# Optimization experiments

Measured on AMD Instinct MI355X. Metric: run time of the kernel, lower is better.

Reference implementation:

```python
import jax, jax.numpy as jnp
import numpy as np

B, C, H, W = 8, 16, 64, 64
O = 32
K = 3
STRIDE = 1
HO = (H - K) // STRIDE + 1  # 62
WO = (W - K) // STRIDE + 1  # 62
BIAS_VAL = 0.1


def setup_inputs() -> dict:
    key = jax.random.key(0)
    k1, k2 = jax.random.split(key)
    x = jax.random.normal(k1, (B, C, H, W), dtype=jnp.float32)
    # per-location weights: (1, O, C, Ho, Wo, K*K) in torch; drop leading 1
    weight = jax.random.normal(k2, (O, C, HO, WO, K * K), dtype=jnp.float32)
    bias = jnp.full((1, O, HO, WO), BIAS_VAL, dtype=jnp.float32)
    return {"x": x, "weight": weight, "bias": bias}


def _extract_patches(x):
    # emulate x.unfold(2,K,S).unfold(3,K,S).reshape(..., K*K)
    # patch index k = ki*K + kj
    patches = [
        x[:, :, ki:ki + (HO - 1) * STRIDE + 1:STRIDE, kj:kj + (WO - 1) * STRIDE + 1:STRIDE]
        for ki in range(K) for kj in range(K)
    ]
    return jnp.stack(patches, axis=-1)  # [B, C, Ho, Wo, K*K]


def reference(x, weight, bias):
    patches = _extract_patches(x)  # [B, C, Ho, Wo, K2]
    # (x.unsqueeze(1) * weight).sum([2, -1]) == contraction over C and K2 per location
    out = jnp.einsum('bchwk,ochwk->bohw', patches, weight)
    return out + bias
```

## Files before the change

### kernel.cpp

```cpp
#include <hip/hip_runtime.h>


#define BB 8
#define CC 16
#define HH 64
#define WW 64
#define OO 32
#define HO 62
#define WO 62
#define NLOC (HO * WO)
#define TOTAL (OO * NLOC)

typedef float f4 __attribute__((ext_vector_type(4)));
typedef float f2 __attribute__((ext_vector_type(2)));

__device__ __forceinline__ void async_f32_to_lds(const float* g, float* l) {
  __builtin_amdgcn_global_load_lds((const __attribute__((address_space(1))) void*)g,
                                   (__attribute__((address_space(3))) void*)l,
                                   4, 0, 0);
}
__device__ __forceinline__ void async_f32x4_to_lds(const float* g, float* l) {
  __builtin_amdgcn_global_load_lds((const __attribute__((address_space(1))) void*)g,
                                   (__attribute__((address_space(3))) void*)l,
                                   16, 0, 0);
}

__global__ __launch_bounds__(256) void lc2d_kernel(
    const float* __restrict__ x, const float* __restrict__ weight,
    const float* __restrict__ bias, float* __restrict__ out) {
  __shared__ __align__(16) float smem[4 * 2 * 576];

  const int tid  = threadIdx.x;
  const int lane = tid & 63;
  const int wave = tid >> 6;
  const int l = lane & 15;
  const int q = lane >> 4;
  const int ho = blockIdx.x % HO;
  const int o  = blockIdx.x / HO;

  float* buf0 = smem + wave * 1152;

  const int colbase = 4 * l;
  const int f2off = (l < 15) ? 4 : -4;

  const float* wbase = weight + (size_t)(o * CC + wave * 4) * (NLOC * 9)
                              + (size_t)ho * (WO * 9);

#define STAGE(SRC, DST)                                              \
  {                                                                  \
    async_f32x4_to_lds((SRC) + lane * 4, (DST));                     \
    async_f32x4_to_lds((SRC) + 256 + lane * 4, (DST) + 256);         \
    if (lane < 46) async_f32_to_lds((SRC) + 512 + lane, (DST) + 512);\
  }

  STAGE(wbase, buf0)

  f4 acc[2];
  acc[0] = (f4)0.f;
  acc[1] = (f4)0.f;

#pragma unroll
  for (int cc = 0; cc < 4; ++cc) {
    const float* cur = buf0 + (cc & 1) * 576;
    float* nxt = buf0 + ((cc + 1) & 1) * 576;
    const int c = wave * 4 + cc;

    __builtin_amdgcn_sched_barrier(0);
    f4 v4[2][3];
    f2 v2[2][3];
#pragma unroll
    for (int bo = 0; bo < 2; ++bo) {
      const float* xb = x + ((size_t)(2 * q + bo) * CC + c) * (HH * WW)
                          + (size_t)ho * WW + colbase;
#pragma unroll
      for (int r = 0; r < 3; ++r) {
        v4[bo][r] = *(const f4*)(xb + r * WW);
        v2[bo][r] = *(const f2*)(xb + r * WW + f2off);
      }
    }
    __builtin_amdgcn_sched_barrier(0);
    if (cc < 3) {
      const float* wg = wbase + (size_t)(cc + 1) * (NLOC * 9);
      STAGE(wg, nxt)
    }
    __builtin_amdgcn_sched_barrier(0);
    if (cc < 3) {
      asm volatile("s_waitcnt vmcnt(15)");
    } else {
      asm volatile("s_waitcnt vmcnt(12)");
    }
    __builtin_amdgcn_sched_barrier(0);

    f4 wq[9];
#pragma unroll
    for (int k = 0; k < 9; ++k)
      wq[k] = *(const f4*)(cur + 36 * l + 4 * k);

#pragma unroll
    for (int bo = 0; bo < 2; ++bo) {
#pragma unroll
      for (int w4 = 0; w4 < 4; ++w4) {
        float s = 0.f;
#pragma unroll
        for (int r = 0; r < 3; ++r) {
#pragma unroll
          for (int j = 0; j < 3; ++j) {
            const int e = w4 + j;
            const int wi = w4 * 9 + r * 3 + j;
            const float xv = (e < 4) ? v4[bo][r][e] : v2[bo][r][e - 4];
            s += xv * wq[wi >> 2][wi & 3];
          }
        }
        acc[bo][w4] += s;
      }
    }
  }
#undef STAGE

#pragma unroll
  for (int bo = 0; bo < 2; ++bo)
    *(f4*)(buf0 + (2 * q + bo) * 64 + colbase) = acc[bo];
  __syncthreads();

  for (int p = tid; p < 512; p += 256) {
    const int b  = p >> 6;
    const int wo = p & 63;
    if (wo < WO) {
      float s = smem[0 * 1152 + p] + smem[1 * 1152 + p]
              + smem[2 * 1152 + p] + smem[3 * 1152 + p];
      const int loc = o * NLOC + ho * WO + wo;
      out[(size_t)b * TOTAL + loc] = s + bias[loc];
    }
  }
}

extern "C" void kernel_launch(void* const* d_in, const int* in_sizes, int n_in,
                              void* d_out, int out_size, void* d_ws, size_t ws_size,
                              hipStream_t stream) {
  const float* x = (const float*)d_in[0];
  const float* w = (const float*)d_in[1];
  const float* bias = (const float*)d_in[2];
  float* out = (float*)d_out;

  hipLaunchKernelGGL(lc2d_kernel, dim3(OO * HO), dim3(256), 0, stream,
                     x, w, bias, out);
}
```

Before: 26.22 us.

## Process four output channels per block to reuse input loads

```diff
diff --git a/kernel.cpp b/kernel.cpp
--- a/kernel.cpp
+++ b/kernel.cpp
@@ -8,6 +8,7 @@
 #define OO 32
 #define HO 62
 #define WO 62
+#define OG 4
 #define NLOC (HO * WO)
 #define TOTAL (OO * NLOC)
 
@@ -28,7 +29,7 @@
 __global__ __launch_bounds__(256) void lc2d_kernel(
     const float* __restrict__ x, const float* __restrict__ weight,
     const float* __restrict__ bias, float* __restrict__ out) {
-  __shared__ __align__(16) float smem[4 * 2 * 576];
+  __shared__ __align__(16) float smem[4 * 2 * OG * 576];
 
   const int tid  = threadIdx.x;
   const int lane = tid & 63;
@@ -36,33 +37,42 @@
   const int l = lane & 15;
   const int q = lane >> 4;
   const int ho = blockIdx.x % HO;
-  const int o  = blockIdx.x / HO;
+  const int og = blockIdx.x / HO;
 
-  float* buf0 = smem + wave * 1152;
+  float* wbuf = smem + wave * (2 * OG * 576);
 
   const int colbase = 4 * l;
   const int f2off = (l < 15) ? 4 : -4;
 
-  const float* wbase = weight + (size_t)(o * CC + wave * 4) * (NLOC * 9)
+  const float* wbase = weight + ((size_t)(og * OG) * CC + wave * 4) * (NLOC * 9)
                               + (size_t)ho * (WO * 9);
 
-#define STAGE(SRC, DST)                                              \
-  {                                                                  \
-    async_f32x4_to_lds((SRC) + lane * 4, (DST));                     \
-    async_f32x4_to_lds((SRC) + 256 + lane * 4, (DST) + 256);         \
-    if (lane < 46) async_f32_to_lds((SRC) + 512 + lane, (DST) + 512);\
+#define STAGE_ROW(SRC, DST)                                            \
+  {                                                                    \
+    async_f32x4_to_lds((SRC) + lane * 4, (DST));                       \
+    async_f32x4_to_lds((SRC) + 256 + lane * 4, (DST) + 256);           \
+    if (lane < 46) async_f32_to_lds((SRC) + 512 + lane, (DST) + 512);  \
+  }
+#define STAGE_BODY(cc, DST)                                            \
+  {                                                                    \
+    _Pragma("unroll")                                                  \
+    for (int oo = 0; oo < OG; ++oo)                                    \
+      STAGE_ROW(wbase + ((size_t)oo * CC + (cc)) * (NLOC * 9),         \
+                (DST) + oo * 576);                                     \
   }
 
-  STAGE(wbase, buf0)
+  STAGE_BODY(0, wbuf)
 
-  f4 acc[2];
-  acc[0] = (f4)0.f;
-  acc[1] = (f4)0.f;
+  f4 acc[2][OG];
+#pragma unroll
+  for (int bo = 0; bo < 2; ++bo)
+#pragma unroll
+    for (int oo = 0; oo < OG; ++oo) acc[bo][oo] = (f4)0.f;
 
 #pragma unroll
   for (int cc = 0; cc < 4; ++cc) {
-    const float* cur = buf0 + (cc & 1) * 576;
-    float* nxt = buf0 + ((cc + 1) & 1) * 576;
+    const float* cur = wbuf + (cc & 1) * (OG * 576);
+    float* nxt = wbuf + ((cc + 1) & 1) * (OG * 576);
     const int c = wave * 4 + cc;
 
     __builtin_amdgcn_sched_barrier(0);
@@ -79,56 +89,60 @@
       }
     }
     __builtin_amdgcn_sched_barrier(0);
-    if (cc < 3) {
-      const float* wg = wbase + (size_t)(cc + 1) * (NLOC * 9);
-      STAGE(wg, nxt)
-    }
+    if (cc < 3) STAGE_BODY(cc + 1, nxt)
     __builtin_amdgcn_sched_barrier(0);
     if (cc < 3) {
-      asm volatile("s_waitcnt vmcnt(15)");
+      asm volatile("s_waitcnt vmcnt(24)");
     } else {
       asm volatile("s_waitcnt vmcnt(12)");
     }
     __builtin_amdgcn_sched_barrier(0);
 
-    f4 wq[9];
 #pragma unroll
-    for (int k = 0; k < 9; ++k)
-      wq[k] = *(const f4*)(cur + 36 * l + 4 * k);
+    for (int oo = 0; oo < OG; ++oo) {
+      f4 wq[9];
+#pragma unroll
+      for (int k = 0; k < 9; ++k)
+        wq[k] = *(const f4*)(cur + oo * 576 + 36 * l + 4 * k);
 
 #pragma unroll
-    for (int bo = 0; bo < 2; ++bo) {
+      for (int bo = 0; bo < 2; ++bo) {
 #pragma unroll
-      for (int w4 = 0; w4 < 4; ++w4) {
-        float s = 0.f;
+        for (int w4 = 0; w4 < 4; ++w4) {
+          float s = 0.f;
 #pragma unroll
-        for (int r = 0; r < 3; ++r) {
+          for (int r = 0; r < 3; ++r) {
 #pragma unroll
-          for (int j = 0; j < 3; ++j) {
-            const int e = w4 + j;
-            const int wi = w4 * 9 + r * 3 + j;
-            const float xv = (e < 4) ? v4[bo][r][e] : v2[bo][r][e - 4];
-            s += xv * wq[wi >> 2][wi & 3];
+            for (int j = 0; j < 3; ++j) {
+              const int e = w4 + j;
+              const int wi = w4 * 9 + r * 3 + j;
+              const float xv = (e < 4) ? v4[bo][r][e] : v2[bo][r][e - 4];
+              s += xv * wq[wi >> 2][wi & 3];
+            }
           }
+          acc[bo][oo][w4] += s;
         }
-        acc[bo][w4] += s;
       }
     }
   }
-#undef STAGE
+#undef STAGE_BODY
+#undef STAGE_ROW
 
 #pragma unroll
-  for (int bo = 0; bo < 2; ++bo)
-    *(f4*)(buf0 + (2 * q + bo) * 64 + colbase) = acc[bo];
+  for (int oo = 0; oo < OG; ++oo)
+#pragma unroll
+    for (int bo = 0; bo < 2; ++bo)
+      *(f4*)(wbuf + (oo * 8 + 2 * q + bo) * 64 + colbase) = acc[bo][oo];
   __syncthreads();
 
-  for (int p = tid; p < 512; p += 256) {
-    const int b  = p >> 6;
+  for (int p = tid; p < OG * 8 * 64; p += 256) {
+    const int oo = p >> 9;
+    const int b  = (p >> 6) & 7;
     const int wo = p & 63;
     if (wo < WO) {
-      float s = smem[0 * 1152 + p] + smem[1 * 1152 + p]
-              + smem[2 * 1152 + p] + smem[3 * 1152 + p];
-      const int loc = o * NLOC + ho * WO + wo;
+      float s = smem[0 * 4608 + p] + smem[1 * 4608 + p]
+              + smem[2 * 4608 + p] + smem[3 * 4608 + p];
+      const int loc = (og * OG + oo) * NLOC + ho * WO + wo;
       out[(size_t)b * TOTAL + loc] = s + bias[loc];
     }
   }
@@ -142,6 +156,6 @@
   const float* bias = (const float*)d_in[2];
   float* out = (float*)d_out;
 
-  hipLaunchKernelGGL(lc2d_kernel, dim3(OO * HO), dim3(256), 0, stream,
+  hipLaunchKernelGGL(lc2d_kernel, dim3((OO / OG) * HO), dim3(256), 0, stream,
                      x, w, bias, out);
 }
```

Result: slower. 30.17 us (+15.0%).

## Split channels over eight waves and stage all weights into LDS up front

Applied to the files above, without the earlier changes.

```diff
diff --git a/kernel.cpp b/kernel.cpp
--- a/kernel.cpp
+++ b/kernel.cpp
@@ -25,10 +25,10 @@
                                    16, 0, 0);
 }
 
-__global__ __launch_bounds__(256) void lc2d_kernel(
+__global__ __launch_bounds__(512) void lc2d_kernel(
     const float* __restrict__ x, const float* __restrict__ weight,
     const float* __restrict__ bias, float* __restrict__ out) {
-  __shared__ __align__(16) float smem[4 * 2 * 576];
+  __shared__ __align__(16) float smem[CC * 576];
 
   const int tid  = threadIdx.x;
   const int lane = tid & 63;
@@ -38,59 +38,59 @@
   const int ho = blockIdx.x % HO;
   const int o  = blockIdx.x / HO;
 
-  float* buf0 = smem + wave * 1152;
-
   const int colbase = 4 * l;
   const int f2off = (l < 15) ? 4 : -4;
 
-  const float* wbase = weight + (size_t)(o * CC + wave * 4) * (NLOC * 9)
-                              + (size_t)ho * (WO * 9);
-
-#define STAGE(SRC, DST)                                              \
-  {                                                                  \
-    async_f32x4_to_lds((SRC) + lane * 4, (DST));                     \
-    async_f32x4_to_lds((SRC) + 256 + lane * 4, (DST) + 256);         \
-    if (lane < 46) async_f32_to_lds((SRC) + 512 + lane, (DST) + 512);\
+  if (wave == 0) {
+    const float* wb = weight + ((size_t)o * CC * NLOC + (size_t)ho * WO) * 9;
+#pragma unroll
+    for (int c = 0; c < CC; ++c) {
+      const float* src = wb + (size_t)c * (NLOC * 9);
+      float* dst = smem + c * 576;
+      async_f32x4_to_lds(src + lane * 4, dst);
+      async_f32x4_to_lds(src + 256 + lane * 4, dst + 256);
+      if (lane < 46) async_f32_to_lds(src + 512 + lane, dst + 512);
+    }
   }
 
-  STAGE(wbase, buf0)
+  const int c0 = 2 * wave;
+  f4 v4[2][3];
+  f2 v2[2][3];
+#pragma unroll
+  for (int bo = 0; bo < 2; ++bo) {
+    const float* xb = x + ((size_t)(2 * q + bo) * CC + c0) * (HH * WW)
+                        + (size_t)ho * WW + colbase;
+#pragma unroll
+    for (int r = 0; r < 3; ++r) {
+      v4[bo][r] = *(const f4*)(xb + r * WW);
+      v2[bo][r] = *(const f2*)(xb + r * WW + f2off);
+    }
+  }
+
+  __syncthreads();
 
   f4 acc[2];
   acc[0] = (f4)0.f;
   acc[1] = (f4)0.f;
 
 #pragma unroll
-  for (int cc = 0; cc < 4; ++cc) {
-    const float* cur = buf0 + (cc & 1) * 576;
-    float* nxt = buf0 + ((cc + 1) & 1) * 576;
-    const int c = wave * 4 + cc;
+  for (int t = 0; t < 2; ++t) {
+    const int c = c0 + t;
 
-    __builtin_amdgcn_sched_barrier(0);
-    f4 v4[2][3];
-    f2 v2[2][3];
+    if (t == 1) {
 #pragma unroll
-    for (int bo = 0; bo < 2; ++bo) {
-      const float* xb = x + ((size_t)(2 * q + bo) * CC + c) * (HH * WW)
-                          + (size_t)ho * WW + colbase;
+      for (int bo = 0; bo < 2; ++bo) {
+        const float* xb = x + ((size_t)(2 * q + bo) * CC + c) * (HH * WW)
+                            + (size_t)ho * WW + colbase;
 #pragma unroll
-      for (int r = 0; r < 3; ++r) {
-        v4[bo][r] = *(const f4*)(xb + r * WW);
-        v2[bo][r] = *(const f2*)(xb + r * WW + f2off);
+        for (int r = 0; r < 3; ++r) {
+          v4[bo][r] = *(const f4*)(xb + r * WW);
+          v2[bo][r] = *(const f2*)(xb + r * WW + f2off);
+        }
       }
     }
-    __builtin_amdgcn_sched_barrier(0);
-    if (cc < 3) {
-      const float* wg = wbase + (size_t)(cc + 1) * (NLOC * 9);
-      STAGE(wg, nxt)
-    }
-    __builtin_amdgcn_sched_barrier(0);
-    if (cc < 3) {
-      asm volatile("s_waitcnt vmcnt(15)");
-    } else {
-      asm volatile("s_waitcnt vmcnt(12)");
-    }
-    __builtin_amdgcn_sched_barrier(0);
 
+    const float* cur = smem + c * 576;
     f4 wq[9];
 #pragma unroll
     for (int k = 0; k < 9; ++k)
@@ -115,19 +115,20 @@
       }
     }
   }
-#undef STAGE
 
 #pragma unroll
   for (int bo = 0; bo < 2; ++bo)
-    *(f4*)(buf0 + (2 * q + bo) * 64 + colbase) = acc[bo];
+    *(f4*)(smem + c0 * 576 + (2 * q + bo) * 64 + colbase) = acc[bo];
   __syncthreads();
 
-  for (int p = tid; p < 512; p += 256) {
-    const int b  = p >> 6;
-    const int wo = p & 63;
+  {
+    const int b  = tid >> 6;
+    const int wo = tid & 63;
     if (wo < WO) {
-      float s = smem[0 * 1152 + p] + smem[1 * 1152 + p]
-              + smem[2 * 1152 + p] + smem[3 * 1152 + p];
+      float s = 0.f;
+#pragma unroll
+      for (int w = 0; w < 8; ++w)
+        s += smem[(2 * w) * 576 + b * 64 + wo];
       const int loc = o * NLOC + ho * WO + wo;
       out[(size_t)b * TOTAL + loc] = s + bias[loc];
     }
@@ -142,6 +143,6 @@
   const float* bias = (const float*)d_in[2];
   float* out = (float*)d_out;
 
-  hipLaunchKernelGGL(lc2d_kernel, dim3(OO * HO), dim3(256), 0, stream,
+  hipLaunchKernelGGL(lc2d_kernel, dim3(OO * HO), dim3(512), 0, stream,
                      x, w, bias, out);
 }
```

Measured after the change: 29.75 us. 1.13x slower.

## Deepen weight staging to triple buffer and prefetch x one channel ahead

Applied to the files above, without the earlier changes.

```diff
diff --git a/kernel.cpp b/kernel.cpp
--- a/kernel.cpp
+++ b/kernel.cpp
@@ -28,7 +28,7 @@
 __global__ __launch_bounds__(256) void lc2d_kernel(
     const float* __restrict__ x, const float* __restrict__ weight,
     const float* __restrict__ bias, float* __restrict__ out) {
-  __shared__ __align__(16) float smem[4 * 2 * 576];
+  __shared__ __align__(16) float smem[4 * 3 * 576];
 
   const int tid  = threadIdx.x;
   const int lane = tid & 63;
@@ -38,7 +38,7 @@
   const int ho = blockIdx.x % HO;
   const int o  = blockIdx.x / HO;
 
-  float* buf0 = smem + wave * 1152;
+  float* wbuf = smem + wave * 1728;
 
   const int colbase = 4 * l;
   const int f2off = (l < 15) ? 4 : -4;
@@ -46,14 +46,32 @@
   const float* wbase = weight + (size_t)(o * CC + wave * 4) * (NLOC * 9)
                               + (size_t)ho * (WO * 9);
 
-#define STAGE(SRC, DST)                                              \
-  {                                                                  \
-    async_f32x4_to_lds((SRC) + lane * 4, (DST));                     \
-    async_f32x4_to_lds((SRC) + 256 + lane * 4, (DST) + 256);         \
-    if (lane < 46) async_f32_to_lds((SRC) + 512 + lane, (DST) + 512);\
+#define STAGE_ROW(SRC, DST)                                            \
+  {                                                                    \
+    async_f32x4_to_lds((SRC) + lane * 4, (DST));                       \
+    async_f32x4_to_lds((SRC) + 256 + lane * 4, (DST) + 256);           \
+    if (lane < 46) async_f32_to_lds((SRC) + 512 + lane, (DST) + 512);  \
+  }
+#define XLOAD(CIDX, S)                                                 \
+  {                                                                    \
+    _Pragma("unroll")                                                  \
+    for (int bo = 0; bo < 2; ++bo) {                                   \
+      const float* xb = x + ((size_t)(2 * q + bo) * CC + (CIDX)) * (HH * WW) \
+                          + (size_t)ho * WW + colbase;                 \
+      _Pragma("unroll")                                                \
+      for (int r = 0; r < 3; ++r) {                                    \
+        xv4[S][bo][r] = *(const f4*)(xb + r * WW);                     \
+        xv2[S][bo][r] = *(const f2*)(xb + r * WW + f2off);             \
+      }                                                                \
+    }                                                                  \
   }
 
-  STAGE(wbase, buf0)
+  f4 xv4[2][2][3];
+  f2 xv2[2][2][3];
+
+  STAGE_ROW(wbase, wbuf)
+  XLOAD(wave * 4, 0)
+  STAGE_ROW(wbase + (size_t)1 * (NLOC * 9), wbuf + 576)
 
   f4 acc[2];
   acc[0] = (f4)0.f;
@@ -61,33 +79,17 @@
 
 #pragma unroll
   for (int cc = 0; cc < 4; ++cc) {
-    const float* cur = buf0 + (cc & 1) * 576;
-    float* nxt = buf0 + ((cc + 1) & 1) * 576;
-    const int c = wave * 4 + cc;
+    const int cs = cc & 1;
+    const int ns = cs ^ 1;
+    const float* cur = wbuf + (cc % 3) * 576;
 
     __builtin_amdgcn_sched_barrier(0);
-    f4 v4[2][3];
-    f2 v2[2][3];
-#pragma unroll
-    for (int bo = 0; bo < 2; ++bo) {
-      const float* xb = x + ((size_t)(2 * q + bo) * CC + c) * (HH * WW)
-                          + (size_t)ho * WW + colbase;
-#pragma unroll
-      for (int r = 0; r < 3; ++r) {
-        v4[bo][r] = *(const f4*)(xb + r * WW);
-        v2[bo][r] = *(const f2*)(xb + r * WW + f2off);
-      }
-    }
-    __builtin_amdgcn_sched_barrier(0);
-    if (cc < 3) {
-      const float* wg = wbase + (size_t)(cc + 1) * (NLOC * 9);
-      STAGE(wg, nxt)
-    }
+    if (cc < 3) XLOAD(wave * 4 + cc + 1, ns)
     __builtin_amdgcn_sched_barrier(0);
     if (cc < 3) {
       asm volatile("s_waitcnt vmcnt(15)");
     } else {
-      asm volatile("s_waitcnt vmcnt(12)");
+      asm volatile("s_waitcnt vmcnt(0)");
     }
     __builtin_amdgcn_sched_barrier(0);
 
@@ -95,6 +97,11 @@
 #pragma unroll
     for (int k = 0; k < 9; ++k)
       wq[k] = *(const f4*)(cur + 36 * l + 4 * k);
+
+    __builtin_amdgcn_sched_barrier(0);
+    if (cc < 2)
+      STAGE_ROW(wbase + (size_t)(cc + 2) * (NLOC * 9), wbuf + ((cc + 2) % 3) * 576)
+    __builtin_amdgcn_sched_barrier(0);
 
 #pragma unroll
     for (int bo = 0; bo < 2; ++bo) {
@@ -107,7 +114,7 @@
           for (int j = 0; j < 3; ++j) {
             const int e = w4 + j;
             const int wi = w4 * 9 + r * 3 + j;
-            const float xv = (e < 4) ? v4[bo][r][e] : v2[bo][r][e - 4];
+            const float xv = (e < 4) ? xv4[cs][bo][r][e] : xv2[cs][bo][r][e - 4];
             s += xv * wq[wi >> 2][wi & 3];
           }
         }
@@ -115,19 +122,20 @@
       }
     }
   }
-#undef STAGE
+#undef XLOAD
+#undef STAGE_ROW
 
 #pragma unroll
   for (int bo = 0; bo < 2; ++bo)
-    *(f4*)(buf0 + (2 * q + bo) * 64 + colbase) = acc[bo];
+    *(f4*)(wbuf + (2 * q + bo) * 64 + colbase) = acc[bo];
   __syncthreads();
 
   for (int p = tid; p < 512; p += 256) {
     const int b  = p >> 6;
     const int wo = p & 63;
     if (wo < WO) {
-      float s = smem[0 * 1152 + p] + smem[1 * 1152 + p]
-              + smem[2 * 1152 + p] + smem[3 * 1152 + p];
+      float s = smem[0 * 1728 + p] + smem[1 * 1728 + p]
+              + smem[2 * 1728 + p] + smem[3 * 1728 + p];
       const int loc = o * NLOC + ho * WO + wo;
       out[(size_t)b * TOTAL + loc] = s + bias[loc];
     }
```

Result: no change. 25.99 us (-0.9%).
